# Kernel tuning notes

Measured on AMD Instinct MI355X. Metric: run time of the kernel, lower is better.

Reference implementation:

```python
import jax, jax.numpy as jnp
import numpy as np

EMBED_DIM = 1024
NUM_HEADS = 16
HEAD_DIM = EMBED_DIM // NUM_HEADS
SCALE = HEAD_DIM ** -0.5


def setup_inputs() -> dict:
    key = jax.random.key(0)
    k1, k2, k3 = jax.random.split(key, 3)
    B, S, E = 2, 2048, EMBED_DIM
    # xavier-uniform-like init scaled down for stability
    x = jax.random.normal(k1, (B, S, E), dtype=jnp.float32)
    w_qkv = jax.random.normal(k2, (3 * E, E), dtype=jnp.float32) * (E ** -0.5)
    w_out = jax.random.normal(k3, (E, E), dtype=jnp.float32) * (E ** -0.5)
    bias_qkv = jnp.zeros((3 * E,), dtype=jnp.float32)
    bias_out = jnp.zeros((E,), dtype=jnp.float32)
    return {"x": x, "w_qkv": w_qkv, "bias_qkv": bias_qkv, "w_out": w_out, "bias_out": bias_out}


def reference(x, w_qkv, bias_qkv, w_out, bias_out):
    B, S, E = x.shape
    H, D = NUM_HEADS, HEAD_DIM
    # fused QKV projection: nn.Linear semantics -> x @ w_qkv.T + bias
    qkv = jnp.einsum('bse,fe->bsf', x, w_qkv) + bias_qkv  # [B,S,3E]
    q, k, v = jnp.split(qkv, 3, axis=-1)
    # reshape to heads
    q = q.reshape(B, S, H, D)
    k = k.reshape(B, S, H, D)
    v = v.reshape(B, S, H, D)
    # scaled dot-product attention (non-causal)
    scores = jnp.einsum('bqhd,bkhd->bhqk', q, k) * SCALE  # [B,H,S,S]
    probs = jax.nn.softmax(scores, axis=-1)
    ctx = jnp.einsum('bhqk,bkhd->bqhd', probs, v).reshape(B, S, E)
    # output projection
    out = jnp.einsum('bse,fe->bsf', ctx, w_out) + bias_out
    return out
```

## Files before the change

### kernel.cpp

```cpp
#include <hip/hip_runtime.h>
#include <hip/hip_bf16.h>


typedef __bf16 bf16_t;
typedef __bf16 bf16x4 __attribute__((ext_vector_type(4)));
typedef __bf16 bf16x8 __attribute__((ext_vector_type(8)));
typedef float f32x4 __attribute__((ext_vector_type(4)));

#define MFMA16(a, b, c) __builtin_amdgcn_mfma_f32_16x16x32_bf16(a, b, c, 0, 0, 0)

static constexpr int Bn = 2;
static constexpr int S = 2048;
static constexpr int E = 1024;
static constexpr int H = 16;
static constexpr int Dh = 64;

__device__ __forceinline__ void gl_lds16(const bf16_t* g, bf16_t* l) {
  __builtin_amdgcn_global_load_lds(
      (const __attribute__((address_space(1))) unsigned int*)g,
      (__attribute__((address_space(3))) unsigned int*)l, 16, 0, 0);
}

__device__ __forceinline__ int detect_fp32(const unsigned short* p) {
  int cnt = 0;
#pragma unroll
  for (int j = 0; j < 32; j++) {
    const int e = (p[j] >> 7) & 0xFF;
    cnt += (e > 140) ? 1 : 0;
  }
  return cnt >= 2;
}

static constexpr int G0 = 4194304 / 8;
static constexpr int G1 = G0 + 3145728 / 8;
static constexpr int G2 = G1 + 3072 / 8;
static constexpr int G3 = G2 + 1048576 / 8;
static constexpr int G4 = G3 + 1024 / 8;

__global__ void convert_all(const void* __restrict__ s0, const void* __restrict__ s1,
                            const void* __restrict__ s2, const void* __restrict__ s3,
                            const void* __restrict__ s4, bf16_t* __restrict__ dst) {
  const int fp32 = detect_fp32((const unsigned short*)s0);
  const int stride = gridDim.x * blockDim.x;
  for (int i = blockIdx.x * blockDim.x + threadIdx.x; i < G4; i += stride) {
    const void* s;
    int off;
    if (i < G0)      { s = s0; off = i; }
    else if (i < G1) { s = s1; off = i - G0; }
    else if (i < G2) { s = s2; off = i - G1; }
    else if (i < G3) { s = s3; off = i - G2; }
    else             { s = s4; off = i - G3; }
    bf16x8 o;
    if (fp32) {
      const float* sp = (const float*)s + off * 8;
#pragma unroll
      for (int j = 0; j < 8; j++) o[j] = (bf16_t)sp[j];
    } else {
      o = *((const bf16x8*)s + off);
    }
    *(bf16x8*)(dst + (size_t)i * 8) = o;
  }
}

__global__ __launch_bounds__(512, 4) void gemm_qkv(
    const bf16_t* __restrict__ X, const bf16_t* __restrict__ W,
    const bf16_t* __restrict__ bias,
    bf16_t* __restrict__ Qo, bf16_t* __restrict__ Ko, bf16_t* __restrict__ Vo) {
  __shared__ bf16_t Alds[2 * 16 * 512];
  __shared__ bf16_t Blds[2 * 24 * 512];
  const int tid = threadIdx.x;
  const int wave = tid >> 6, lane = tid & 63;
  const int lr = lane & 15, quad = lane >> 4;
  const int wm = wave >> 2, wn = wave & 3;
  const int m0 = blockIdx.y * 128, n0 = blockIdx.x * 192;
  constexpr int Kd = 1024;

  auto STAGE = [&](int ao, int bo, int k0) {
#pragma unroll
    for (int i = 0; i < 2; i++) {
      const int fb = wave * 2 + i;
      const int mt = fb >> 1, kc = fb & 1;
      gl_lds16(X + (size_t)(m0 + mt * 16 + lr) * Kd + k0 + kc * 32 + quad * 8,
               &Alds[ao + fb * 512]);
    }
#pragma unroll
    for (int i = 0; i < 3; i++) {
      const int fb = wave * 3 + i;
      const int nt = fb >> 1, kc = fb & 1;
      gl_lds16(W + (size_t)(n0 + nt * 16 + lr) * Kd + k0 + kc * 32 + quad * 8,
               &Blds[bo + fb * 512]);
    }
  };

  f32x4 acc[4][3] = {};

  STAGE(0, 0, 0);
  __syncthreads();

  int buf = 0;
#pragma unroll 2
  for (int k0 = 0; k0 < Kd; k0 += 64) {
    const int ao = buf * 8192, bo = buf * 12288;
    if (k0 + 64 < Kd) STAGE(ao ^ 8192, bo ^ 12288, k0 + 64);
#pragma unroll
    for (int kc = 0; kc < 2; kc++) {
      bf16x8 af[4], bfr[3];
#pragma unroll
      for (int mt = 0; mt < 4; mt++)
        af[mt] = *(const bf16x8*)&Alds[ao + ((wm * 4 + mt) * 2 + kc) * 512 + lane * 8];
#pragma unroll
      for (int nt = 0; nt < 3; nt++)
        bfr[nt] = *(const bf16x8*)&Blds[bo + ((wn * 3 + nt) * 2 + kc) * 512 + lane * 8];
#pragma unroll
      for (int mt = 0; mt < 4; mt++)
#pragma unroll
        for (int nt = 0; nt < 3; nt++)
          acc[mt][nt] = MFMA16(af[mt], bfr[nt], acc[mt][nt]);
    }
    __syncthreads();
    buf ^= 1;
  }

  const int m0w = m0 + wm * 64, n0w = n0 + wn * 48;
#pragma unroll
  for (int nt = 0; nt < 3; nt++) {
    const int col = n0w + nt * 16 + lr;
    const float bs = (float)bias[col];
    const int which = col >> 10;
    const int e = col & 1023;
    const int h = e >> 6, d = e & 63;
#pragma unroll
    for (int mt = 0; mt < 4; mt++) {
      const int row0 = m0w + mt * 16 + quad * 4;
      const int b = row0 >> 11, s0 = row0 & 2047;
      if (which == 2) {
        bf16x4 v4;
#pragma unroll
        for (int r = 0; r < 4; r++) v4[r] = (bf16_t)(acc[mt][nt][r] + bs);
        *(bf16x4*)&Vo[((size_t)((b * H + h) * Dh + d)) * S + s0] = v4;
      } else {
        bf16_t* dst = (which == 0) ? Qo : Ko;
#pragma unroll
        for (int r = 0; r < 4; r++)
          dst[((size_t)((b * H + h) * S + (s0 + r))) * Dh + d] =
              (bf16_t)(acc[mt][nt][r] + bs);
      }
    }
  }
}

__global__ __launch_bounds__(256, 2) void attn_kernel(
    const bf16_t* __restrict__ Q, const bf16_t* __restrict__ K,
    const bf16_t* __restrict__ Vt, bf16_t* __restrict__ CTX) {
  __shared__ bf16_t Kl[2 * 8 * 512];
  __shared__ bf16_t Vl[2 * 8 * 512];
  __shared__ bf16_t Psh[4 * 32 * 64];

  const int tid = threadIdx.x;
  const int wave = tid >> 6, lane = tid & 63;
  const int lr = lane & 15, quad = lane >> 4;

  const int blk = blockIdx.x;
  const int bh = blk & 31;
  const int qt = blk >> 5;
  const int b = bh >> 4, h = bh & 15;

  const bf16_t* Qb = Q + (size_t)bh * S * Dh;
  const bf16_t* Kb = K + (size_t)bh * S * Dh;
  const bf16_t* Vb = Vt + (size_t)bh * Dh * S;

  const int q0 = qt * 128 + wave * 32;

  bf16x8 aq[2][2];
#pragma unroll
  for (int mt = 0; mt < 2; mt++)
#pragma unroll
    for (int kc = 0; kc < 2; kc++) {
      bf16x8 t = *(const bf16x8*)(Qb + (size_t)(q0 + mt * 16 + lr) * Dh +
                                  kc * 32 + quad * 8);
#pragma unroll
      for (int j = 0; j < 8; j++) t[j] = (bf16_t)((float)t[j] * 0.125f);
      aq[mt][kc] = t;
    }

  bf16x8 ones;
#pragma unroll
  for (int j = 0; j < 8; j++) ones[j] = (bf16_t)1.0f;

  bf16_t* pw = &Psh[wave * 32 * 64];
  const int xl = (lr & 7) << 3;

  const bf16_t* kg = Kb + (size_t)(wave * 16 + lr) * Dh + quad * 8;
  const bf16_t* vg = Vb + (size_t)(wave * 16 + lr) * S + quad * 8;

  f32x4 O[2][4] = {};
  f32x4 lacc[2] = {};

  {
    gl_lds16(kg, &Kl[(wave * 2 + 0) * 512]);
    gl_lds16(kg + 32, &Kl[(wave * 2 + 1) * 512]);
    gl_lds16(vg, &Vl[(wave * 2 + 0) * 512]);
    gl_lds16(vg + 32, &Vl[(wave * 2 + 1) * 512]);
  }
  __syncthreads();

  int buf = 0;
#pragma unroll 2
  for (int sk0 = 0; sk0 < S; sk0 += 64) {
    const int bb = buf * 4096;
    const int nb = (buf ^ 1) * 4096;

    if (sk0 + 64 < S) {
      const int skn = sk0 + 64;
      gl_lds16(kg + (size_t)skn * Dh, &Kl[nb + (wave * 2 + 0) * 512]);
      gl_lds16(kg + (size_t)skn * Dh + 32, &Kl[nb + (wave * 2 + 1) * 512]);
      gl_lds16(vg + skn, &Vl[nb + (wave * 2 + 0) * 512]);
      gl_lds16(vg + skn + 32, &Vl[nb + (wave * 2 + 1) * 512]);
    }

    f32x4 scT[2][4];
#pragma unroll
    for (int nt = 0; nt < 4; nt++) {
      const bf16x8 k0f = *(const bf16x8*)&Kl[bb + (nt * 2 + 0) * 512 + lane * 8];
      const bf16x8 k1f = *(const bf16x8*)&Kl[bb + (nt * 2 + 1) * 512 + lane * 8];
#pragma unroll
      for (int mt = 0; mt < 2; mt++) {
        f32x4 z = {};
        z = MFMA16(k0f, aq[mt][0], z);
        scT[mt][nt] = MFMA16(k1f, aq[mt][1], z);
      }
    }

    bf16x8 vf[4][2];
#pragma unroll
    for (int dt = 0; dt < 4; dt++) {
      vf[dt][0] = *(const bf16x8*)&Vl[bb + (dt * 2 + 0) * 512 + lane * 8];
      vf[dt][1] = *(const bf16x8*)&Vl[bb + (dt * 2 + 1) * 512 + lane * 8];
    }

#pragma unroll
    for (int mt = 0; mt < 2; mt++) {
      bf16_t* pr = &pw[(mt * 16 + lr) * 64];
#pragma unroll
      for (int nt = 0; nt < 4; nt++) {
        bf16x4 p4;
#pragma unroll
        for (int r = 0; r < 4; r++) p4[r] = (bf16_t)__expf(scT[mt][nt][r]);
        *(bf16x4*)&pr[(nt * 16 + quad * 4) ^ xl] = p4;
      }
    }

#pragma unroll
    for (int mt = 0; mt < 2; mt++) {
      const bf16x8 ap0 =
          *(const bf16x8*)&pw[(mt * 16 + lr) * 64 + ((quad * 8) ^ xl)];
      const bf16x8 ap1 =
          *(const bf16x8*)&pw[(mt * 16 + lr) * 64 + ((quad * 8 + 32) ^ xl)];
      lacc[mt] = MFMA16(ap0, ones, lacc[mt]);
      lacc[mt] = MFMA16(ap1, ones, lacc[mt]);
#pragma unroll
      for (int dt = 0; dt < 4; dt++) {
        O[mt][dt] = MFMA16(ap0, vf[dt][0], O[mt][dt]);
        O[mt][dt] = MFMA16(ap1, vf[dt][1], O[mt][dt]);
      }
    }

    __syncthreads();
    buf ^= 1;
  }

#pragma unroll
  for (int mt = 0; mt < 2; mt++) {
    float rl[4];
#pragma unroll
    for (int r = 0; r < 4; r++) rl[r] = 1.0f / lacc[mt][r];
#pragma unroll
    for (int dt = 0; dt < 4; dt++)
#pragma unroll
      for (int r = 0; r < 4; r++) {
        const int qrow = q0 + mt * 16 + quad * 4 + r;
        CTX[(size_t)(b * S + qrow) * E + h * 64 + dt * 16 + lr] =
            (bf16_t)(O[mt][dt][r] * rl[r]);
      }
  }
}

__global__ __launch_bounds__(256) void gemm_out(
    const bf16_t* __restrict__ X, const bf16_t* __restrict__ W,
    const bf16_t* __restrict__ bias, void* __restrict__ Out,
    const void* __restrict__ xin) {
  __shared__ bf16_t Alds[8 * 512];
  __shared__ bf16_t Blds[16 * 512];
  const int tid = threadIdx.x;
  const int wave = tid >> 6, lane = tid & 63;
  const int lr = lane & 15, quad = lane >> 4;
  const int wm = wave >> 1, wn = wave & 1;
  const int m0 = blockIdx.y * 64, n0 = blockIdx.x * 128;
  constexpr int Kd = 1024;

  f32x4 acc[2][4] = {};
  for (int k0 = 0; k0 < Kd; k0 += 64) {
    __syncthreads();
#pragma unroll
    for (int kc = 0; kc < 2; kc++)
      gl_lds16(X + (size_t)(m0 + wave * 16 + lr) * Kd + k0 + kc * 32 + quad * 8,
               &Alds[(wave * 2 + kc) * 512]);
#pragma unroll
    for (int i = 0; i < 2; i++) {
      const int nt = wave * 2 + i;
#pragma unroll
      for (int kc = 0; kc < 2; kc++)
        gl_lds16(W + (size_t)(n0 + nt * 16 + lr) * Kd + k0 + kc * 32 + quad * 8,
                 &Blds[(nt * 2 + kc) * 512]);
    }
    __syncthreads();
#pragma unroll
    for (int kc = 0; kc < 2; kc++) {
      bf16x8 af[2], bfr[4];
#pragma unroll
      for (int mt = 0; mt < 2; mt++)
        af[mt] = *(const bf16x8*)&Alds[((wm * 2 + mt) * 2 + kc) * 512 + lane * 8];
#pragma unroll
      for (int nt = 0; nt < 4; nt++)
        bfr[nt] = *(const bf16x8*)&Blds[((wn * 4 + nt) * 2 + kc) * 512 + lane * 8];
#pragma unroll
      for (int mt = 0; mt < 2; mt++)
#pragma unroll
        for (int nt = 0; nt < 4; nt++)
          acc[mt][nt] = MFMA16(af[mt], bfr[nt], acc[mt][nt]);
    }
  }

  const int fp32 = detect_fp32((const unsigned short*)xin);
  const int m0w = m0 + wm * 32, n0w = n0 + wn * 64;
#pragma unroll
  for (int nt = 0; nt < 4; nt++) {
    const int col = n0w + nt * 16 + lr;
    const float bs = (float)bias[col];
#pragma unroll
    for (int mt = 0; mt < 2; mt++) {
#pragma unroll
      for (int r = 0; r < 4; r++) {
        const int row = m0w + mt * 16 + quad * 4 + r;
        const float v = acc[mt][nt][r] + bs;
        if (fp32)
          ((float*)Out)[(size_t)row * E + col] = v;
        else
          ((bf16_t*)Out)[(size_t)row * E + col] = (bf16_t)v;
      }
    }
  }
}

extern "C" void kernel_launch(void* const* d_in, const int* in_sizes, int n_in,
                              void* d_out, int out_size, void* d_ws, size_t ws_size,
                              hipStream_t stream) {
  const void* x = d_in[0];
  const void* w_qkv = d_in[1];
  const void* b_qkv = d_in[2];
  const void* w_out = d_in[3];
  const void* b_out = d_in[4];

  bf16_t* base = (bf16_t*)d_ws;
  const int N_X = Bn * S * E;
  const int N_WQ = 3 * E * E;
  const int N_BQ = 3 * E;
  const int N_WO = E * E;
  const int N_BO = E;
  bf16_t* xb = base;
  bf16_t* wqb = xb + N_X;
  bf16_t* bqb = wqb + N_WQ;
  bf16_t* wob = bqb + N_BQ;
  bf16_t* bob = wob + N_WO;
  const size_t QKV_ELEMS = (size_t)Bn * H * S * Dh;
  bf16_t* Qw = bob + N_BO;
  bf16_t* Kw = Qw + QKV_ELEMS;
  bf16_t* Vw = Kw + QKV_ELEMS;
  bf16_t* CTXw = Vw + QKV_ELEMS;

  convert_all<<<1024, 256, 0, stream>>>(x, w_qkv, b_qkv, w_out, b_out, xb);
  gemm_qkv<<<dim3(3 * E / 192, Bn * S / 128), 512, 0, stream>>>(xb, wqb, bqb, Qw, Kw, Vw);
  attn_kernel<<<16 * Bn * H, 256, 0, stream>>>(Qw, Kw, Vw, CTXw);
  gemm_out<<<dim3(E / 128, Bn * S / 64), 256, 0, stream>>>(CTXw, wob, bob, d_out, x);
}
```

Before: 207.6 us.

## Double-buffer output GEMM and widen attention key tile to 128

The attention kernel now stages 128 keys per iteration instead of 64, processing two 64-key halves per loop trip, so it hits half as many block barriers and issues larger prefetches. The output projection GEMM switches to a 128x64 tile and gains double-buffered LDS prefetch of the next K slice, replacing the two barriers per step with one. Both changes increase LDS usage, which may lower occupancy. gemm_out also gets a 2-blocks-per-CU launch bound.

```diff
diff --git a/kernel.cpp b/kernel.cpp
--- a/kernel.cpp
+++ b/kernel.cpp
@@ -152,8 +152,8 @@
 __global__ __launch_bounds__(256, 2) void attn_kernel(
     const bf16_t* __restrict__ Q, const bf16_t* __restrict__ K,
     const bf16_t* __restrict__ Vt, bf16_t* __restrict__ CTX) {
-  __shared__ bf16_t Kl[2 * 8 * 512];
-  __shared__ bf16_t Vl[2 * 8 * 512];
+  __shared__ bf16_t Kl[2 * 16 * 512];
+  __shared__ bf16_t Vl[2 * 16 * 512];
   __shared__ bf16_t Psh[4 * 32 * 64];
 
   const int tid = threadIdx.x;
@@ -190,78 +190,81 @@
   bf16_t* pw = &Psh[wave * 32 * 64];
   const int xl = (lr & 7) << 3;
 
-  const bf16_t* kg = Kb + (size_t)(wave * 16 + lr) * Dh + quad * 8;
-  const bf16_t* vg = Vb + (size_t)(wave * 16 + lr) * S + quad * 8;
+  const bf16_t* kgl = Kb + (size_t)lr * Dh + quad * 8;
+  const bf16_t* vgl = Vb + (size_t)lr * S + quad * 8;
+
+  auto STAGE = [&](int bb, int sk0) {
+#pragma unroll
+    for (int i = 0; i < 4; i++) {
+      const int fb = wave * 4 + i;
+      const int kt = fb >> 1, kc = fb & 1;
+      gl_lds16(kgl + (size_t)(sk0 + kt * 16) * Dh + kc * 32, &Kl[bb + fb * 512]);
+      const int dt = fb >> 2, hk = fb & 3;
+      gl_lds16(vgl + (size_t)(dt * 16) * S + sk0 + hk * 32, &Vl[bb + fb * 512]);
+    }
+  };
 
   f32x4 O[2][4] = {};
   f32x4 lacc[2] = {};
 
-  {
-    gl_lds16(kg, &Kl[(wave * 2 + 0) * 512]);
-    gl_lds16(kg + 32, &Kl[(wave * 2 + 1) * 512]);
-    gl_lds16(vg, &Vl[(wave * 2 + 0) * 512]);
-    gl_lds16(vg + 32, &Vl[(wave * 2 + 1) * 512]);
-  }
+  STAGE(0, 0);
   __syncthreads();
 
   int buf = 0;
 #pragma unroll 2
-  for (int sk0 = 0; sk0 < S; sk0 += 64) {
-    const int bb = buf * 4096;
-    const int nb = (buf ^ 1) * 4096;
-
-    if (sk0 + 64 < S) {
-      const int skn = sk0 + 64;
-      gl_lds16(kg + (size_t)skn * Dh, &Kl[nb + (wave * 2 + 0) * 512]);
-      gl_lds16(kg + (size_t)skn * Dh + 32, &Kl[nb + (wave * 2 + 1) * 512]);
-      gl_lds16(vg + skn, &Vl[nb + (wave * 2 + 0) * 512]);
-      gl_lds16(vg + skn + 32, &Vl[nb + (wave * 2 + 1) * 512]);
-    }
-
-    f32x4 scT[2][4];
-#pragma unroll
-    for (int nt = 0; nt < 4; nt++) {
-      const bf16x8 k0f = *(const bf16x8*)&Kl[bb + (nt * 2 + 0) * 512 + lane * 8];
-      const bf16x8 k1f = *(const bf16x8*)&Kl[bb + (nt * 2 + 1) * 512 + lane * 8];
+  for (int sk0 = 0; sk0 < S; sk0 += 128) {
+    const int bb = buf * 8192;
+
+    if (sk0 + 128 < S) STAGE(bb ^ 8192, sk0 + 128);
+
+#pragma unroll
+    for (int hh = 0; hh < 2; hh++) {
+      f32x4 scT[2][4];
+#pragma unroll
+      for (int nt = 0; nt < 4; nt++) {
+        const int kt = hh * 4 + nt;
+        const bf16x8 k0f = *(const bf16x8*)&Kl[bb + (kt * 2 + 0) * 512 + lane * 8];
+        const bf16x8 k1f = *(const bf16x8*)&Kl[bb + (kt * 2 + 1) * 512 + lane * 8];
+#pragma unroll
+        for (int mt = 0; mt < 2; mt++) {
+          f32x4 z = {};
+          z = MFMA16(k0f, aq[mt][0], z);
+          scT[mt][nt] = MFMA16(k1f, aq[mt][1], z);
+        }
+      }
+
+      bf16x8 vf[4][2];
+#pragma unroll
+      for (int dt = 0; dt < 4; dt++) {
+        vf[dt][0] = *(const bf16x8*)&Vl[bb + (dt * 4 + hh * 2 + 0) * 512 + lane * 8];
+        vf[dt][1] = *(const bf16x8*)&Vl[bb + (dt * 4 + hh * 2 + 1) * 512 + lane * 8];
+      }
+
 #pragma unroll
       for (int mt = 0; mt < 2; mt++) {
-        f32x4 z = {};
-        z = MFMA16(k0f, aq[mt][0], z);
-        scT[mt][nt] = MFMA16(k1f, aq[mt][1], z);
-      }
-    }
-
-    bf16x8 vf[4][2];
-#pragma unroll
-    for (int dt = 0; dt < 4; dt++) {
-      vf[dt][0] = *(const bf16x8*)&Vl[bb + (dt * 2 + 0) * 512 + lane * 8];
-      vf[dt][1] = *(const bf16x8*)&Vl[bb + (dt * 2 + 1) * 512 + lane * 8];
-    }
-
-#pragma unroll
-    for (int mt = 0; mt < 2; mt++) {
-      bf16_t* pr = &pw[(mt * 16 + lr) * 64];
-#pragma unroll
-      for (int nt = 0; nt < 4; nt++) {
-        bf16x4 p4;
-#pragma unroll
-        for (int r = 0; r < 4; r++) p4[r] = (bf16_t)__expf(scT[mt][nt][r]);
-        *(bf16x4*)&pr[(nt * 16 + quad * 4) ^ xl] = p4;
-      }
-    }
-
-#pragma unroll
-    for (int mt = 0; mt < 2; mt++) {
-      const bf16x8 ap0 =
-          *(const bf16x8*)&pw[(mt * 16 + lr) * 64 + ((quad * 8) ^ xl)];
-      const bf16x8 ap1 =
-          *(const bf16x8*)&pw[(mt * 16 + lr) * 64 + ((quad * 8 + 32) ^ xl)];
-      lacc[mt] = MFMA16(ap0, ones, lacc[mt]);
-      lacc[mt] = MFMA16(ap1, ones, lacc[mt]);
-#pragma unroll
-      for (int dt = 0; dt < 4; dt++) {
-        O[mt][dt] = MFMA16(ap0, vf[dt][0], O[mt][dt]);
-        O[mt][dt] = MFMA16(ap1, vf[dt][1], O[mt][dt]);
+        bf16_t* pr = &pw[(mt * 16 + lr) * 64];
+#pragma unroll
+        for (int nt = 0; nt < 4; nt++) {
+          bf16x4 p4;
+#pragma unroll
+          for (int r = 0; r < 4; r++) p4[r] = (bf16_t)__expf(scT[mt][nt][r]);
+          *(bf16x4*)&pr[(nt * 16 + quad * 4) ^ xl] = p4;
+        }
+      }
+
+#pragma unroll
+      for (int mt = 0; mt < 2; mt++) {
+        const bf16x8 ap0 =
+            *(const bf16x8*)&pw[(mt * 16 + lr) * 64 + ((quad * 8) ^ xl)];
+        const bf16x8 ap1 =
+            *(const bf16x8*)&pw[(mt * 16 + lr) * 64 + ((quad * 8 + 32) ^ xl)];
+        lacc[mt] = MFMA16(ap0, ones, lacc[mt]);
+        lacc[mt] = MFMA16(ap1, ones, lacc[mt]);
+#pragma unroll
+        for (int dt = 0; dt < 4; dt++) {
+          O[mt][dt] = MFMA16(ap0, vf[dt][0], O[mt][dt]);
+          O[mt][dt] = MFMA16(ap1, vf[dt][1], O[mt][dt]);
+        }
       }
     }
 
@@ -285,60 +288,73 @@
   }
 }
 
-__global__ __launch_bounds__(256) void gemm_out(
+__global__ __launch_bounds__(256, 2) void gemm_out(
     const bf16_t* __restrict__ X, const bf16_t* __restrict__ W,
     const bf16_t* __restrict__ bias, void* __restrict__ Out,
     const void* __restrict__ xin) {
-  __shared__ bf16_t Alds[8 * 512];
-  __shared__ bf16_t Blds[16 * 512];
+  __shared__ bf16_t Alds[2 * 16 * 512];
+  __shared__ bf16_t Blds[2 * 8 * 512];
   const int tid = threadIdx.x;
   const int wave = tid >> 6, lane = tid & 63;
   const int lr = lane & 15, quad = lane >> 4;
   const int wm = wave >> 1, wn = wave & 1;
-  const int m0 = blockIdx.y * 64, n0 = blockIdx.x * 128;
+  const int m0 = blockIdx.y * 128, n0 = blockIdx.x * 64;
   constexpr int Kd = 1024;
 
-  f32x4 acc[2][4] = {};
+  auto STAGE = [&](int ao, int bo, int k0) {
+#pragma unroll
+    for (int i = 0; i < 4; i++) {
+      const int fb = wave * 4 + i;
+      const int mt = fb >> 1, kc = fb & 1;
+      gl_lds16(X + (size_t)(m0 + mt * 16 + lr) * Kd + k0 + kc * 32 + quad * 8,
+               &Alds[ao + fb * 512]);
+    }
+#pragma unroll
+    for (int i = 0; i < 2; i++) {
+      const int fb = wave * 2 + i;
+      const int nt = fb >> 1, kc = fb & 1;
+      gl_lds16(W + (size_t)(n0 + nt * 16 + lr) * Kd + k0 + kc * 32 + quad * 8,
+               &Blds[bo + fb * 512]);
+    }
+  };
+
+  f32x4 acc[4][2] = {};
+
+  STAGE(0, 0, 0);
+  __syncthreads();
+
+  int buf = 0;
+#pragma unroll 2
   for (int k0 = 0; k0 < Kd; k0 += 64) {
+    const int ao = buf * 8192, bo = buf * 4096;
+    if (k0 + 64 < Kd) STAGE(ao ^ 8192, bo ^ 4096, k0 + 64);
+#pragma unroll
+    for (int kc = 0; kc < 2; kc++) {
+      bf16x8 af[4], bfr[2];
+#pragma unroll
+      for (int mt = 0; mt < 4; mt++)
+        af[mt] = *(const bf16x8*)&Alds[ao + ((wm * 4 + mt) * 2 + kc) * 512 + lane * 8];
+#pragma unroll
+      for (int nt = 0; nt < 2; nt++)
+        bfr[nt] = *(const bf16x8*)&Blds[bo + ((wn * 2 + nt) * 2 + kc) * 512 + lane * 8];
+#pragma unroll
+      for (int mt = 0; mt < 4; mt++)
+#pragma unroll
+        for (int nt = 0; nt < 2; nt++)
+          acc[mt][nt] = MFMA16(af[mt], bfr[nt], acc[mt][nt]);
+    }
     __syncthreads();
-#pragma unroll
-    for (int kc = 0; kc < 2; kc++)
-      gl_lds16(X + (size_t)(m0 + wave * 16 + lr) * Kd + k0 + kc * 32 + quad * 8,
-               &Alds[(wave * 2 + kc) * 512]);
-#pragma unroll
-    for (int i = 0; i < 2; i++) {
-      const int nt = wave * 2 + i;
-#pragma unroll
-      for (int kc = 0; kc < 2; kc++)
-        gl_lds16(W + (size_t)(n0 + nt * 16 + lr) * Kd + k0 + kc * 32 + quad * 8,
-                 &Blds[(nt * 2 + kc) * 512]);
-    }
-    __syncthreads();
-#pragma unroll
-    for (int kc = 0; kc < 2; kc++) {
-      bf16x8 af[2], bfr[4];
-#pragma unroll
-      for (int mt = 0; mt < 2; mt++)
-        af[mt] = *(const bf16x8*)&Alds[((wm * 2 + mt) * 2 + kc) * 512 + lane * 8];
-#pragma unroll
-      for (int nt = 0; nt < 4; nt++)
-        bfr[nt] = *(const bf16x8*)&Blds[((wn * 4 + nt) * 2 + kc) * 512 + lane * 8];
-#pragma unroll
-      for (int mt = 0; mt < 2; mt++)
-#pragma unroll
-        for (int nt = 0; nt < 4; nt++)
-          acc[mt][nt] = MFMA16(af[mt], bfr[nt], acc[mt][nt]);
-    }
+    buf ^= 1;
   }
 
   const int fp32 = detect_fp32((const unsigned short*)xin);
-  const int m0w = m0 + wm * 32, n0w = n0 + wn * 64;
-#pragma unroll
-  for (int nt = 0; nt < 4; nt++) {
+  const int m0w = m0 + wm * 64, n0w = n0 + wn * 32;
+#pragma unroll
+  for (int nt = 0; nt < 2; nt++) {
     const int col = n0w + nt * 16 + lr;
     const float bs = (float)bias[col];
 #pragma unroll
-    for (int mt = 0; mt < 2; mt++) {
+    for (int mt = 0; mt < 4; mt++) {
 #pragma unroll
       for (int r = 0; r < 4; r++) {
         const int row = m0w + mt * 16 + quad * 4 + r;
@@ -381,5 +397,5 @@
   convert_all<<<1024, 256, 0, stream>>>(x, w_qkv, b_qkv, w_out, b_out, xb);
   gemm_qkv<<<dim3(3 * E / 192, Bn * S / 128), 512, 0, stream>>>(xb, wqb, bqb, Qw, Kw, Vw);
   attn_kernel<<<16 * Bn * H, 256, 0, stream>>>(Qw, Kw, Vw, CTXw);
-  gemm_out<<<dim3(E / 128, Bn * S / 64), 256, 0, stream>>>(CTXw, wob, bob, d_out, x);
-}
+  gemm_out<<<dim3(E / 64, Bn * S / 128), 256, 0, stream>>>(CTXw, wob, bob, d_out, x);
+}
```

Measured after the change: 207.0 us. About the same (-0.3%).
